# Performance work log

Hardware: AMD Instinct MI355X
Metric: run time of the kernel (lower is better)

## Reference

```python
import jax, jax.numpy as jnp
import numpy as np

MC_SAMPLES = 32  # k neighbors
BIG = 1e8


def _swish(x):
    return x * jax.nn.sigmoid(x)


def setup_inputs() -> dict:
    key = jax.random.key(0)
    ks = jax.random.split(key, 8)
    bs, n, d, c = 8, 1024, 3, 64
    cmco_ci, hid = 16, 32
    abq_pairs = jax.random.normal(ks[0], (bs, n, n, d), dtype=jnp.float32)
    vals = jax.random.normal(ks[1], (bs, n, c), dtype=jnp.float32)
    mask = jnp.ones((bs, n), dtype=bool)
    s = 0.1
    return {
        "abq_pairs": abq_pairs,
        "vals": vals,
        "mask": mask,
        "W1": jax.random.normal(ks[2], (d, hid), dtype=jnp.float32) * s,
        "b1": jnp.zeros((hid,), jnp.float32),
        "W2": jax.random.normal(ks[3], (hid, hid), dtype=jnp.float32) * s,
        "b2": jnp.zeros((hid,), jnp.float32),
        "W3": jax.random.normal(ks[4], (hid, cmco_ci), dtype=jnp.float32) * s,
        "b3": jnp.zeros((cmco_ci,), jnp.float32),
        "Wl": jax.random.normal(ks[5], (c * cmco_ci, c), dtype=jnp.float32) * s,
        "bl": jnp.zeros((c,), jnp.float32),
    }


def reference(abq_pairs, vals, mask, W1, b1, W2, b2, W3, b3, Wl, bl):
    bs, n, _, d = abq_pairs.shape
    c = vals.shape[-1]
    k = min(MC_SAMPLES, n)

    # --- extract_neighborhood (knn branch, ds_frac=1 so queries = all points) ---
    # Trivial group distance = norm over last dim of abq pairs: (bs,n,n)
    dists = jnp.linalg.norm(abq_pairs, axis=-1)
    dists = jnp.where(mask[:, None, :], dists, BIG)
    _, nbhd_idx = jax.lax.top_k(-dists, k)  # smallest-k -> (bs, n, k)

    # gather neighbor pairwise embeddings: (bs, n, k, d)
    nbhd_abq = jnp.take_along_axis(abq_pairs, nbhd_idx[..., None], axis=2)
    # gather neighbor values and mask per batch: (bs, n, k, c), (bs, n, k)
    nbhd_vals = jax.vmap(lambda v, i: v[i])(vals, nbhd_idx)
    nbhd_mask = jax.vmap(lambda m, i: m[i])(mask, nbhd_idx) & mask[:, :, None]

    h = _swish(nbhd_abq @ W1 + b1)
    h = _swish(h @ W2 + b2)
    penult_kernel_weights = _swish(h @ W3 + b3)  # (bs, n, k, 16)

    # --- masked weighted aggregation (generalized PointConv trick) ---
    mW = jnp.where(nbhd_mask[..., None], penult_kernel_weights, 0.0)
    mV = jnp.where(nbhd_mask[..., None], nbhd_vals, 0.0)
    # vals^T @ weights -> (bs, n, c, 16) -> (bs, n, c*16)
    partial = jnp.einsum("bmkc,bmkp->bmcp", mV, mW).reshape(bs, n, -1)
    convolved = partial @ Wl + bl  # (bs, n, c)

    # zero out invalid query points
    return jnp.where(mask[..., None], convolved, 0.0)
```

## Files before the change

kernel.cpp:

```cpp
#include <hip/hip_runtime.h>
#include <math.h>


#define NPTS 1024
#define KNB  32
#define CCH  64
#define HID  32
#define PCH  16

#define OFF_PACK  196608
#define OFF_NB    4456448
#define PACKN     1808

__device__ __forceinline__ float swishf(float x) {
    return x * __builtin_amdgcn_rcpf(1.0f + __expf(-x));
}

__global__ __launch_bounds__(256) void lieconv_pack(
    const float* __restrict__ W1, const float* __restrict__ b1,
    const float* __restrict__ W2, const float* __restrict__ b2,
    const float* __restrict__ W3, const float* __restrict__ b3,
    float* __restrict__ ws)
{
    const int tid = threadIdx.x;
    float* pack = ws + OFF_PACK;
    for (int idx = tid; idx < PACKN; idx += 256) {
        float v;
        if (idx < 128) {
            int i4 = idx >> 4, rem = idx & 15, r = rem >> 2, u = rem & 3;
            v = (r < 3) ? W1[r * 32 + i4 * 4 + u] : b1[i4 * 4 + u];
        } else if (idx < 1792) {
            int oi = idx - 128;
            int o = oi / 52, t = oi - o * 52;
            if (t < 32)       v = W2[t * 32 + o];
            else if (t < 48)  v = W3[o * 16 + (t - 32)];
            else if (t == 48) v = b2[o];
            else              v = 0.0f;
        } else {
            v = b3[idx - 1792];
        }
        pack[idx] = v;
    }
}

__global__ __launch_bounds__(256, 8) void lieconv_knn(
    const float* __restrict__ abq, unsigned short* __restrict__ sel_out,
    float* __restrict__ nbbuf)
{
    __shared__ int s_cand[4][64];
    const int tid  = threadIdx.x;
    const int lane = tid & 63;
    const int w    = tid >> 6;
    const int row  = blockIdx.x * 4 + w;
    const float* __restrict__ rowp = abq + (size_t)row * (NPTS * 3);

    float kf[16];
#pragma unroll
    for (int q = 0; q < 16; ++q) {
        int j = q * 64 + lane;
        float x = rowp[j * 3 + 0];
        float y = rowp[j * 3 + 1];
        float z = rowp[j * 3 + 2];
        kf[q] = fmaf(x, x, fmaf(y, y, z * z));
    }
    float kmax = kf[0];
#pragma unroll
    for (int q = 1; q < 16; ++q) kmax = fmaxf(kmax, kf[q]);
#pragma unroll
    for (int off = 32; off > 0; off >>= 1)
        kmax = fmaxf(kmax, __shfl_xor(kmax, off, 64));

    float lo = 0.0f, hi = kmax * 1.000001f + 1e-30f, T = hi;
    for (int it = 0; it < 28; ++it) {
        float mid = 0.5f * (lo + hi);
        int c = 0;
#pragma unroll
        for (int q = 0; q < 16; ++q)
            c += __popcll(__ballot(kf[q] < mid));
        if (c < KNB)      lo = mid;
        else if (c > 40)  hi = mid;
        else { T = mid; break; }
        T = hi;
    }
    float Tcut = T * 1.000001f;

    const unsigned long long lmask = (1ull << lane) - 1ull;
    int base = 0;
#pragma unroll
    for (int q = 0; q < 16; ++q) {
        bool p = kf[q] < Tcut;
        unsigned long long mk = __ballot(p);
        int pos = base + __popcll(mk & lmask);
        if (p && pos < 64) s_cand[w][pos] = q * 64 + lane;
        base += __popcll(mk);
    }
    int ncand = (base < 64) ? base : 64;

    unsigned long long ci = ~0ull;
    int ji = 0x7fffffff;
    if (lane < ncand) {
        ji = s_cand[w][lane];
        double x = (double)rowp[ji * 3 + 0];
        double y = (double)rowp[ji * 3 + 1];
        double z = (double)rowp[ji * 3 + 2];
        double ki = (x * x + y * y) + z * z;
        ci = ((unsigned long long)__double_as_longlong(ki) & ~1023ull) | (unsigned)ji;
    }
    int rank = 0;
#pragma unroll
    for (int t = 0; t < 64; ++t) {
        unsigned long long ct = __shfl(ci, t, 64);
        rank += (ct < ci) ? 1 : 0;
    }
    bool sel = (lane < ncand) && (rank < KNB);
    unsigned long long mk = __ballot(sel);
    if (sel) {
        int pos = (int)((size_t)row * KNB) + __popcll(mk & lmask);
        sel_out[pos] = (unsigned short)ji;
        float* nb = nbbuf + (size_t)pos * 3;
        nb[0] = rowp[ji * 3 + 0];
        nb[1] = rowp[ji * 3 + 1];
        nb[2] = rowp[ji * 3 + 2];
    }
}

#define WVS 20

__global__ __launch_bounds__(256, 3) void lieconv_tail(
    const float* __restrict__ vals, const unsigned short* __restrict__ sel,
    const float* __restrict__ ws_ro, const float* __restrict__ Wl,
    const float* __restrict__ bl, float* __restrict__ out)
{
    __shared__ __align__(16) float s_mem[8 * 1024 + 256 * WVS];
    float* s_part = s_mem;
    float* s_pack = s_mem;
    float* s_wv   = s_mem + 8192;
    float* s_red  = s_mem + 8192;

    const int tid  = threadIdx.x;
    const int lane = tid & 63;
    const int w    = tid >> 6;
    const size_t r0 = (size_t)blockIdx.x * 8;

#pragma unroll
    for (int u = 0; u < 8; ++u) {
        int idx = u * 256 + tid;
        if (idx < PACKN) s_pack[idx] = ws_ro[OFF_PACK + idx];
    }
    __syncthreads();

    {
        const size_t P = (size_t)blockIdx.x * 256 + tid;
        const float* __restrict__ nb = ws_ro + OFF_NB + P * 3;
        float x = nb[0], y = nb[1], z = nb[2];

        const float4* __restrict__ w1p = (const float4*)s_pack;
        const float4* __restrict__ opk = (const float4*)s_pack + 32;
        const float4* __restrict__ b3q = (const float4*)(s_pack + 1792);

        float h1[32];
#pragma unroll
        for (int i4 = 0; i4 < 8; ++i4) {
            float4 qa = w1p[i4 * 4 + 0];
            float4 qb = w1p[i4 * 4 + 1];
            float4 qc = w1p[i4 * 4 + 2];
            float4 qd = w1p[i4 * 4 + 3];
            h1[i4 * 4 + 0] = swishf(fmaf(x, qa.x, fmaf(y, qb.x, fmaf(z, qc.x, qd.x))));
            h1[i4 * 4 + 1] = swishf(fmaf(x, qa.y, fmaf(y, qb.y, fmaf(z, qc.y, qd.y))));
            h1[i4 * 4 + 2] = swishf(fmaf(x, qa.z, fmaf(y, qb.z, fmaf(z, qc.z, qd.z))));
            h1[i4 * 4 + 3] = swishf(fmaf(x, qa.w, fmaf(y, qb.w, fmaf(z, qc.w, qd.w))));
        }

        float wv[16];
        {
            float4 q0 = b3q[0], q1 = b3q[1], q2 = b3q[2], q3 = b3q[3];
            wv[0]=q0.x; wv[1]=q0.y; wv[2]=q0.z; wv[3]=q0.w;
            wv[4]=q1.x; wv[5]=q1.y; wv[6]=q1.z; wv[7]=q1.w;
            wv[8]=q2.x; wv[9]=q2.y; wv[10]=q2.z; wv[11]=q2.w;
            wv[12]=q3.x; wv[13]=q3.y; wv[14]=q3.z; wv[15]=q3.w;
        }
#pragma unroll
        for (int o = 0; o < 32; ++o) {
            const float4* q = opk + o * 13;
            float acc = q[12].x;
#pragma unroll
            for (int n = 0; n < 8; ++n) {
                float4 qq = q[n];
                acc = fmaf(h1[n * 4 + 0], qq.x, acc);
                acc = fmaf(h1[n * 4 + 1], qq.y, acc);
                acc = fmaf(h1[n * 4 + 2], qq.z, acc);
                acc = fmaf(h1[n * 4 + 3], qq.w, acc);
            }
            float h2 = swishf(acc);
#pragma unroll
            for (int n = 0; n < 4; ++n) {
                float4 qq = q[8 + n];
                wv[n * 4 + 0] = fmaf(h2, qq.x, wv[n * 4 + 0]);
                wv[n * 4 + 1] = fmaf(h2, qq.y, wv[n * 4 + 1]);
                wv[n * 4 + 2] = fmaf(h2, qq.z, wv[n * 4 + 2]);
                wv[n * 4 + 3] = fmaf(h2, qq.w, wv[n * 4 + 3]);
            }
        }
        float* wo = &s_wv[tid * WVS];
#pragma unroll
        for (int n = 0; n < 4; ++n)
            *(float4*)&wo[n * 4] = make_float4(swishf(wv[n * 4 + 0]), swishf(wv[n * 4 + 1]),
                                               swishf(wv[n * 4 + 2]), swishf(wv[n * 4 + 3]));
    }
    __syncthreads();

    const int p4    = (lane & 3) * 4;
    const int cbase = lane >> 2;
#pragma unroll
    for (int rr = 0; rr < 2; ++rr) {
        const int lr = w * 2 + rr;
        const size_t R = r0 + lr;
        const float* __restrict__ valsb = vals + (R >> 10) * (size_t)(NPTS * CCH);
        const unsigned short* __restrict__ selr = sel + R * KNB;

        int jj_l = (int)selr[lane & 31];

        float acc[4][4];
#pragma unroll
        for (int it = 0; it < 4; ++it)
#pragma unroll
            for (int e = 0; e < 4; ++e) acc[it][e] = 0.0f;

#pragma unroll 8
        for (int kk = 0; kk < KNB; ++kk) {
            int jj = __shfl(jj_l, kk, 64);
            float4 wq = *(const float4*)&s_wv[(lr * 32 + kk) * WVS + p4];
            const float* vr = valsb + (size_t)jj * CCH + cbase;
#pragma unroll
            for (int it = 0; it < 4; ++it) {
                float v = vr[16 * it];
                acc[it][0] = fmaf(v, wq.x, acc[it][0]);
                acc[it][1] = fmaf(v, wq.y, acc[it][1]);
                acc[it][2] = fmaf(v, wq.z, acc[it][2]);
                acc[it][3] = fmaf(v, wq.w, acc[it][3]);
            }
        }
#pragma unroll
        for (int it = 0; it < 4; ++it) {
            int c = cbase + 16 * it;
            *(float4*)&s_part[lr * 1024 + c * PCH + p4] =
                make_float4(acc[it][0], acc[it][1], acc[it][2], acc[it][3]);
        }
    }
    __syncthreads();

    {
        const int c = lane;
        float accr[8];
#pragma unroll
        for (int r = 0; r < 8; ++r) accr[r] = 0.0f;

        const int k0 = w * 256;
        for (int kq = k0; kq < k0 + 256; kq += 4) {
            float w0 = Wl[(size_t)(kq + 0) * 64 + c];
            float w1 = Wl[(size_t)(kq + 1) * 64 + c];
            float w2 = Wl[(size_t)(kq + 2) * 64 + c];
            float w3 = Wl[(size_t)(kq + 3) * 64 + c];
#pragma unroll
            for (int r = 0; r < 8; ++r) {
                float4 pr = *(const float4*)&s_part[r * 1024 + kq];
                accr[r] = fmaf(pr.x, w0,
                          fmaf(pr.y, w1,
                          fmaf(pr.z, w2,
                          fmaf(pr.w, w3, accr[r]))));
            }
        }
#pragma unroll
        for (int r = 0; r < 8; ++r)
            s_red[(w * 8 + r) * 64 + c] = accr[r];
    }
    __syncthreads();

#pragma unroll
    for (int half = 0; half < 2; ++half) {
        int idx = half * 256 + tid;
        int r = idx >> 6, c = idx & 63;
        float s = s_red[(0 * 8 + r) * 64 + c] + s_red[(1 * 8 + r) * 64 + c]
                + s_red[(2 * 8 + r) * 64 + c] + s_red[(3 * 8 + r) * 64 + c];
        out[(r0 + r) * 64 + c] = s + bl[c];
    }
}

extern "C" void kernel_launch(void* const* d_in, const int* in_sizes, int n_in,
                              void* d_out, int out_size, void* d_ws, size_t ws_size,
                              hipStream_t stream)
{
    const float* abq  = (const float*)d_in[0];
    const float* vals = (const float*)d_in[1];
    const float* W1 = (const float*)d_in[3];
    const float* b1 = (const float*)d_in[4];
    const float* W2 = (const float*)d_in[5];
    const float* b2 = (const float*)d_in[6];
    const float* W3 = (const float*)d_in[7];
    const float* b3 = (const float*)d_in[8];
    const float* Wl = (const float*)d_in[9];
    const float* bl = (const float*)d_in[10];
    float* out = (float*)d_out;

    float* ws = (float*)d_ws;
    unsigned short* sel = (unsigned short*)d_ws;
    float* nbbuf = ws + OFF_NB;

    hipLaunchKernelGGL(lieconv_pack, dim3(1), dim3(256), 0, stream,
                       W1, b1, W2, b2, W3, b3, ws);
    hipLaunchKernelGGL(lieconv_knn, dim3(2048), dim3(256), 0, stream,
                       abq, sel, nbbuf);
    hipLaunchKernelGGL(lieconv_tail, dim3(1024), dim3(256), 0, stream,
                       vals, sel, ws, Wl, bl, out);
}
```

Baseline: 245.7 us.

## Run final Wl projection on bf16 MFMA with pre-packed weights and swizzled LDS

```diff
diff --git a/kernel.cpp b/kernel.cpp
--- a/kernel.cpp
+++ b/kernel.cpp
@@ -8,38 +8,65 @@
 #define HID  32
 #define PCH  16
 
-#define OFF_PACK  196608
-#define OFF_NB    4456448
-#define PACKN     1808
+#define OFF_PACK    196608
+#define OFF_NB      4456448
+#define PACKN       1808
+#define OFF_WLB_U16 262144
+
+typedef __bf16        bf16x8 __attribute__((ext_vector_type(8)));
+typedef float         f32x4  __attribute__((ext_vector_type(4)));
+typedef unsigned int  uint4v __attribute__((ext_vector_type(4)));
 
 __device__ __forceinline__ float swishf(float x) {
     return x * __builtin_amdgcn_rcpf(1.0f + __expf(-x));
+}
+
+__device__ __forceinline__ unsigned bf16rne(float f) {
+    unsigned u = __float_as_uint(f);
+    return (u + 0x7fffu + ((u >> 16) & 1u)) >> 16;
 }
 
 __global__ __launch_bounds__(256) void lieconv_pack(
     const float* __restrict__ W1, const float* __restrict__ b1,
     const float* __restrict__ W2, const float* __restrict__ b2,
     const float* __restrict__ W3, const float* __restrict__ b3,
-    float* __restrict__ ws)
+    const float* __restrict__ Wl, float* __restrict__ ws)
 {
     const int tid = threadIdx.x;
-    float* pack = ws + OFF_PACK;
-    for (int idx = tid; idx < PACKN; idx += 256) {
-        float v;
-        if (idx < 128) {
-            int i4 = idx >> 4, rem = idx & 15, r = rem >> 2, u = rem & 3;
-            v = (r < 3) ? W1[r * 32 + i4 * 4 + u] : b1[i4 * 4 + u];
-        } else if (idx < 1792) {
-            int oi = idx - 128;
-            int o = oi / 52, t = oi - o * 52;
-            if (t < 32)       v = W2[t * 32 + o];
-            else if (t < 48)  v = W3[o * 16 + (t - 32)];
-            else if (t == 48) v = b2[o];
-            else              v = 0.0f;
-        } else {
-            v = b3[idx - 1792];
-        }
-        pack[idx] = v;
+    if (blockIdx.x == 0) {
+        float* pack = ws + OFF_PACK;
+        for (int idx = tid; idx < PACKN; idx += 256) {
+            float v;
+            if (idx < 128) {
+                int i4 = idx >> 4, rem = idx & 15, r = rem >> 2, u = rem & 3;
+                v = (r < 3) ? W1[r * 32 + i4 * 4 + u] : b1[i4 * 4 + u];
+            } else if (idx < 1792) {
+                int oi = idx - 128;
+                int o = oi / 52, t = oi - o * 52;
+                if (t < 32)       v = W2[t * 32 + o];
+                else if (t < 48)  v = W3[o * 16 + (t - 32)];
+                else if (t == 48) v = b2[o];
+                else              v = 0.0f;
+            } else {
+                v = b3[idx - 1792];
+            }
+            pack[idx] = v;
+        }
+    } else {
+        const int t   = (blockIdx.x - 1) * 256 + tid;
+        const int g   = t >> 6, l = t & 63;
+        const int k0  = (g >> 2) * 32 + ((l >> 4) << 3);
+        const int col = ((g & 3) << 4) + (l & 15);
+        unsigned us[8];
+#pragma unroll
+        for (int j = 0; j < 8; ++j)
+            us[j] = bf16rne(Wl[(size_t)(k0 + j) * 64 + col]);
+        uint4 pk;
+        pk.x = us[0] | (us[1] << 16);
+        pk.y = us[2] | (us[3] << 16);
+        pk.z = us[4] | (us[5] << 16);
+        pk.w = us[6] | (us[7] << 16);
+        *(uint4*)((unsigned short*)ws + OFF_WLB_U16 + (size_t)t * 8) = pk;
     }
 }
 
@@ -126,16 +153,15 @@
 
 #define WVS 20
 
-__global__ __launch_bounds__(256, 3) void lieconv_tail(
+__global__ __launch_bounds__(256, 4) void lieconv_tail(
     const float* __restrict__ vals, const unsigned short* __restrict__ sel,
     const float* __restrict__ ws_ro, const float* __restrict__ Wl,
     const float* __restrict__ bl, float* __restrict__ out)
 {
-    __shared__ __align__(16) float s_mem[8 * 1024 + 256 * WVS];
-    float* s_part = s_mem;
+    __shared__ __align__(16) float s_mem[4096 + 256 * WVS];
     float* s_pack = s_mem;
-    float* s_wv   = s_mem + 8192;
-    float* s_red  = s_mem + 8192;
+    float* s_wv   = s_mem + 4096;
+    char*  spb    = (char*)s_mem;
 
     const int tid  = threadIdx.x;
     const int lane = tid & 63;
@@ -240,49 +266,48 @@
                 acc[it][3] = fmaf(v, wq.w, acc[it][3]);
             }
         }
+        const unsigned xr = (unsigned)((lr & 7) << 4);
 #pragma unroll
         for (int it = 0; it < 4; ++it) {
             int c = cbase + 16 * it;
-            *(float4*)&s_part[lr * 1024 + c * PCH + p4] =
-                make_float4(acc[it][0], acc[it][1], acc[it][2], acc[it][3]);
+            unsigned kb  = (unsigned)(c * 32 + p4 * 2);
+            unsigned off = (unsigned)(lr * 2048) + (kb ^ xr);
+            uint2 pkv;
+            pkv.x = bf16rne(acc[it][0]) | (bf16rne(acc[it][1]) << 16);
+            pkv.y = bf16rne(acc[it][2]) | (bf16rne(acc[it][3]) << 16);
+            *(uint2*)(spb + off) = pkv;
         }
     }
     __syncthreads();
 
     {
-        const int c = lane;
-        float accr[8];
-#pragma unroll
-        for (int r = 0; r < 8; ++r) accr[r] = 0.0f;
-
-        const int k0 = w * 256;
-        for (int kq = k0; kq < k0 + 256; kq += 4) {
-            float w0 = Wl[(size_t)(kq + 0) * 64 + c];
-            float w1 = Wl[(size_t)(kq + 1) * 64 + c];
-            float w2 = Wl[(size_t)(kq + 2) * 64 + c];
-            float w3 = Wl[(size_t)(kq + 3) * 64 + c];
-#pragma unroll
-            for (int r = 0; r < 8; ++r) {
-                float4 pr = *(const float4*)&s_part[r * 1024 + kq];
-                accr[r] = fmaf(pr.x, w0,
-                          fmaf(pr.y, w1,
-                          fmaf(pr.z, w2,
-                          fmaf(pr.w, w3, accr[r]))));
-            }
-        }
-#pragma unroll
-        for (int r = 0; r < 8; ++r)
-            s_red[(w * 8 + r) * 64 + c] = accr[r];
-    }
-    __syncthreads();
-
-#pragma unroll
-    for (int half = 0; half < 2; ++half) {
-        int idx = half * 256 + tid;
-        int r = idx >> 6, c = idx & 63;
-        float s = s_red[(0 * 8 + r) * 64 + c] + s_red[(1 * 8 + r) * 64 + c]
-                + s_red[(2 * 8 + r) * 64 + c] + s_red[(3 * 8 + r) * 64 + c];
-        out[(r0 + r) * 64 + c] = s + bl[c];
+        const int arow = lane & 15;
+        const int kgrp = lane >> 4;
+        const bf16x8* __restrict__ wlb8 =
+            (const bf16x8*)((const unsigned short*)ws_ro + OFF_WLB_U16) + (w * 64 + lane);
+
+        uint4v zz = {0u, 0u, 0u, 0u};
+        const bf16x8 a0 = __builtin_bit_cast(bf16x8, zz);
+        f32x4 acc = {0.0f, 0.0f, 0.0f, 0.0f};
+
+        const unsigned x     = (unsigned)((arow & 7) << 4);
+        const unsigned abase = (unsigned)(arow * 2048) + ((unsigned)(kgrp * 16) ^ (x & 48u));
+        const unsigned xl    = x & 64u;
+#pragma unroll 8
+        for (int s = 0; s < 32; ++s) {
+            bf16x8 a = a0;
+            if (arow < 8)
+                a = *(const bf16x8*)(spb + (abase + (((unsigned)(s * 64)) ^ xl)));
+            bf16x8 b = wlb8[(size_t)s * 256];
+            acc = __builtin_amdgcn_mfma_f32_16x16x32_bf16(a, b, acc, 0, 0, 0);
+        }
+        if (kgrp < 2) {
+            const int cc   = w * 16 + arow;
+            const float bias = bl[cc];
+#pragma unroll
+            for (int r4 = 0; r4 < 4; ++r4)
+                out[(r0 + kgrp * 4 + r4) * 64 + cc] = acc[r4] + bias;
+        }
     }
 }
 
@@ -306,8 +331,8 @@
     unsigned short* sel = (unsigned short*)d_ws;
     float* nbbuf = ws + OFF_NB;
 
-    hipLaunchKernelGGL(lieconv_pack, dim3(1), dim3(256), 0, stream,
-                       W1, b1, W2, b2, W3, b3, ws);
+    hipLaunchKernelGGL(lieconv_pack, dim3(33), dim3(256), 0, stream,
+                       W1, b1, W2, b2, W3, b3, Wl, ws);
     hipLaunchKernelGGL(lieconv_knn, dim3(2048), dim3(256), 0, stream,
                        abq, sel, nbbuf);
     hipLaunchKernelGGL(lieconv_tail, dim3(1024), dim3(256), 0, stream,
```

New measurement: 223.0 us. 1.1x faster.
